# Kernel tuning notes

Hardware: AMD Instinct MI355X
Metric: run time of the kernel (lower is better)

The kernel has to match this reference:

```python
import jax, jax.numpy as jnp
import numpy as np

SEQ_LEN, BATCH, DIM = 4096, 16, 1024
MIN_SPAN = 8
MAX_SPAN = 200
LN_EPS = 1e-5

def _linear(x, w, b):
    return x @ w.T + b

def _layernorm(x, g, b):
    mu = jnp.mean(x, axis=-1, keepdims=True)
    var = jnp.var(x, axis=-1, keepdims=True)
    return (x - mu) * jax.lax.rsqrt(var + LN_EPS) * g + b

def _relevance_pool(hist, context, decay, w1, b1, w2, b2):
    # hist: [L,B,D], context: [B,D]; batched version of the per-sample torch loop
    L = hist.shape[0]
    ctx = jnp.broadcast_to(context[None], (L,) + context.shape)
    comb = jnp.concatenate([hist, ctx], axis=-1)                      # [L,B,2D]
    h = jax.nn.gelu(_linear(comb, w1, b1), approximate=False)
    scores = _linear(h, w2, b2)[..., 0]                               # [L,B]
    pos = jnp.arange(L, dtype=hist.dtype)
    dec = decay ** (L - 1 - pos)                                      # temporal decay, newest=1
    w = jax.nn.softmax(scores + jnp.log(dec + 1e-8)[:, None], axis=0) # softmax over time
    return jnp.einsum('lb,lbd->bd', w, hist)                          # [B,D]

def setup_inputs() -> dict:
    key = jax.random.key(0)
    ks = jax.random.split(key, 12)
    D, H = DIM, DIM // 2
    s = lambda k, shape, fan: jax.random.normal(k, shape, jnp.float32) * (1.0 / np.sqrt(fan))
    return {
        'features': jax.random.normal(ks[0], (SEQ_LEN, BATCH, D), jnp.float32),
        'w_sp1': s(ks[1], (H, D), D), 'b_sp1': jnp.zeros((H,), jnp.float32),
        'w_sp2': s(ks[2], (3, H), H), 'b_sp2': jnp.zeros((3,), jnp.float32),
        'w_rs1': s(ks[3], (H, 2 * D), 2 * D), 'b_rs1': jnp.zeros((H,), jnp.float32),
        'w_rs2': s(ks[4], (1, H), H), 'b_rs2': jnp.zeros((1,), jnp.float32),
        'decay_local': jnp.array(0.9, jnp.float32),
        'decay_global': jnp.array(0.8, jnp.float32),
        'w_ff': s(ks[5], (D, 2 * D), 2 * D), 'b_ff': jnp.zeros((D,), jnp.float32),
        'ln_ff_g': jnp.ones((D,), jnp.float32), 'ln_ff_b': jnp.zeros((D,), jnp.float32),
        'w_gate': s(ks[6], (D, D), D), 'b_gate': jnp.zeros((D,), jnp.float32),
        'ln_g': jnp.ones((D,), jnp.float32), 'ln_b': jnp.zeros((D,), jnp.float32),
    }

def reference(features, w_sp1, b_sp1, w_sp2, b_sp2, w_rs1, b_rs1, w_rs2, b_rs2,
              decay_local, decay_global, w_ff, b_ff, ln_ff_g, ln_ff_b,
              w_gate, b_gate, ln_g, ln_b):
    S, B, D = features.shape
    context = jnp.mean(features, axis=0)                              # [B,D]
    sp_h = jax.nn.gelu(_linear(context, w_sp1, b_sp1), approximate=False)
    span_weights = jax.nn.softmax(_linear(sp_h, w_sp2, b_sp2), axis=-1)  # [B,3]

    local_span = min(MIN_SPAN * 4, S)                                 # 32
    local_hist = features[-local_span:]                               # [32,B,D]
    local_feat = _relevance_pool(local_hist, context, decay_local,
                                 w_rs1, b_rs1, w_rs2, b_rs2)          # [B,D]

    step = max(1, S // 32) if S > 32 else 1
    global_hist = features[::step]                                    # [~32,B,D]
    global_feat = _relevance_pool(global_hist, context, decay_global,
                                  w_rs1, b_rs1, w_rs2, b_rs2)         # [B,D]

    combined = jnp.concatenate([local_feat * span_weights[:, 1:2],
                                global_feat * span_weights[:, 2:3]], axis=-1)  # [B,2D]
    fused = _layernorm(jax.nn.gelu(_linear(combined, w_ff, b_ff), approximate=False),
                       ln_ff_g, ln_ff_b)                              # [B,D]

    fused_expanded = jnp.broadcast_to(fused[None], (S, B, D))
    gate = jax.nn.sigmoid(_linear(fused_expanded, w_gate, b_gate))    # [S,B,D]
    output = _layernorm(fused_expanded * gate + features, ln_g, ln_b)

    attention_weights = jnp.full((S, B), 1.0 / S, dtype=features.dtype)
    return output, attention_weights
```

## Files before the change

kernel.cpp:

```cpp
#include <hip/hip_runtime.h>
#include <hip/hip_bf16.h>

#define S_LEN 4096
#define BATCH 16
#define DIM 1024
#define HDIM 512
#define LPOOL 32
#define NCOL (BATCH * DIM)
#define NCOL4 (NCOL / 4)
#define SCHUNK 64
#define ROWS_PER_CHUNK (S_LEN / SCHUNK)
#define LN_EPS 1e-5f

__device__ __forceinline__ float gelu_exact(float x) {
    return 0.5f * x * (1.0f + erff(x * 0.70710678118654752440f));
}

__device__ __forceinline__ float wave_reduce_sum(float v) {
    #pragma unroll
    for (int off = 32; off > 0; off >>= 1) v += __shfl_down(v, off);
    return v;
}

__global__ void __launch_bounds__(256) k_colsum(const float* __restrict__ f,
                                                float* __restrict__ part) {
    int cb = blockIdx.x;
    int sc = blockIdx.y;
    int t  = threadIdx.x;
    int c4 = cb * 256 + t;
    const float4* f4 = (const float4*)f;
    float4 acc = make_float4(0.f, 0.f, 0.f, 0.f);
    int base = sc * ROWS_PER_CHUNK;
    #pragma unroll 4
    for (int i = 0; i < ROWS_PER_CHUNK; ++i) {
        float4 v = f4[(size_t)(base + i) * NCOL4 + c4];
        acc.x += v.x; acc.y += v.y; acc.z += v.z; acc.w += v.w;
    }
    ((float4*)part)[(size_t)sc * NCOL4 + c4] = acc;
}

__global__ void __launch_bounds__(256) k_ctx_reduce(const float* __restrict__ part,
                                                    float* __restrict__ context) {
    int c = blockIdx.x * 256 + threadIdx.x;
    float s = 0.f;
    #pragma unroll 8
    for (int k = 0; k < SCHUNK; ++k) s += part[(size_t)k * NCOL + c];
    context[c] = s * (1.0f / (float)S_LEN);
}

__global__ void k_transpose(const float* __restrict__ w, float* __restrict__ wT) {
    __shared__ float tile[32][33];
    int jt = blockIdx.x * 32;
    int dt = blockIdx.y * 32;
    int tx = threadIdx.x & 31, ty = threadIdx.x >> 5;
    #pragma unroll
    for (int i = 0; i < 32; i += 8)
        tile[ty + i][tx] = w[(size_t)(jt + ty + i) * 2048 + dt + tx];
    __syncthreads();
    #pragma unroll
    for (int i = 0; i < 32; i += 8)
        wT[(size_t)(dt + ty + i) * 512 + jt + tx] = tile[tx][ty + i];
}

__global__ void k_sph(const float* __restrict__ ctx, const float* __restrict__ w1,
                      const float* __restrict__ b1, float* __restrict__ sph) {
    int wid = blockIdx.x * 4 + (threadIdx.x >> 6);
    int lane = threadIdx.x & 63;
    int b = wid >> 9;
    int j = wid & 511;
    const float4* x4 = (const float4*)(ctx + (size_t)b * DIM);
    const float4* w4 = (const float4*)(w1 + (size_t)j * DIM);
    float s = 0.f;
    #pragma unroll
    for (int i = 0; i < 4; ++i) {
        float4 a = x4[lane + i * 64], w = w4[lane + i * 64];
        s += a.x * w.x + a.y * w.y + a.z * w.z + a.w * w.w;
    }
    s = wave_reduce_sum(s);
    if (lane == 0) sph[b * HDIM + j] = gelu_exact(s + b1[j]);
}

__global__ void k_span(const float* __restrict__ sph, const float* __restrict__ w2,
                       const float* __restrict__ b2, float* __restrict__ spanw) {
    int b = blockIdx.x, lane = threadIdx.x;
    float vals[3];
    #pragma unroll
    for (int k = 0; k < 3; ++k) {
        const float4* x4 = (const float4*)(sph + (size_t)b * HDIM);
        const float4* w4 = (const float4*)(w2 + (size_t)k * HDIM);
        float s = 0.f;
        #pragma unroll
        for (int i = 0; i < 2; ++i) {
            float4 a = x4[lane + i * 64], w = w4[lane + i * 64];
            s += a.x * w.x + a.y * w.y + a.z * w.z + a.w * w.w;
        }
        s = wave_reduce_sum(s);
        vals[k] = s;
    }
    if (lane == 0) {
        float l0 = vals[0] + b2[0], l1 = vals[1] + b2[1], l2 = vals[2] + b2[2];
        float m = fmaxf(l0, fmaxf(l1, l2));
        float e0 = expf(l0 - m), e1 = expf(l1 - m), e2 = expf(l2 - m);
        float inv = 1.0f / (e0 + e1 + e2);
        spanw[b * 3 + 0] = e0 * inv;
        spanw[b * 3 + 1] = e1 * inv;
        spanw[b * 3 + 2] = e2 * inv;
    }
}

__global__ void k_ctxpart(const float* __restrict__ ctx, const float* __restrict__ wrs1,
                          const float* __restrict__ brs1, float* __restrict__ cpart) {
    int wid = blockIdx.x * 4 + (threadIdx.x >> 6);
    int lane = threadIdx.x & 63;
    int b = wid >> 9;
    int j = wid & 511;
    const float4* x4 = (const float4*)(ctx + (size_t)b * DIM);
    const float4* w4 = (const float4*)(wrs1 + (size_t)j * 2048 + 1024);
    float s = 0.f;
    #pragma unroll
    for (int i = 0; i < 4; ++i) {
        float4 a = x4[lane + i * 64], w = w4[lane + i * 64];
        s += a.x * w.x + a.y * w.y + a.z * w.z + a.w * w.w;
    }
    s = wave_reduce_sum(s);
    if (lane == 0) cpart[b * HDIM + j] = s + brs1[j];
}

__global__ void __launch_bounds__(256) k_poolh(const float* __restrict__ feat,
                                               const float* __restrict__ wT,
                                               const float* __restrict__ cpart,
                                               float* __restrict__ hws) {
    int pl = blockIdx.x;
    int p = pl >> 5, l = pl & 31;
    int jq = blockIdx.y;
    int s = (p == 0) ? (S_LEN - LPOOL + l) : (l * (S_LEN / 32));
    __shared__ float hist[BATCH * DIM];
    const float4* src4 = (const float4*)(feat + (size_t)s * NCOL);
    float4* h4 = (float4*)hist;
    #pragma unroll
    for (int i = 0; i < 16; ++i) h4[threadIdx.x + i * 256] = src4[threadIdx.x + i * 256];
    __syncthreads();
    int lane = threadIdx.x & 63;
    int b0 = (threadIdx.x >> 6) * 4;
    int j0 = jq * 128 + lane * 2;
    float acc[4][2];
    #pragma unroll
    for (int k = 0; k < 4; ++k) {
        acc[k][0] = cpart[(b0 + k) * HDIM + j0];
        acc[k][1] = cpart[(b0 + k) * HDIM + j0 + 1];
    }
    #pragma unroll 4
    for (int d = 0; d < DIM; ++d) {
        float2 w = *(const float2*)&wT[(size_t)d * HDIM + j0];
        #pragma unroll
        for (int k = 0; k < 4; ++k) {
            float h = hist[(b0 + k) * DIM + d];
            acc[k][0] += h * w.x;
            acc[k][1] += h * w.y;
        }
    }
    #pragma unroll
    for (int k = 0; k < 4; ++k) {
        int b = b0 + k;
        float2 o = make_float2(gelu_exact(acc[k][0]), gelu_exact(acc[k][1]));
        *(float2*)&hws[(((size_t)pl) * BATCH + b) * HDIM + j0] = o;
    }
}

__global__ void k_pool_finish(const float* __restrict__ feat, const float* __restrict__ hws,
                              const float* __restrict__ wrs2, const float* __restrict__ brs2,
                              const float* __restrict__ spanw, const float* __restrict__ dl,
                              const float* __restrict__ dg, float* __restrict__ combined) {
    int p = blockIdx.x >> 4, b = blockIdx.x & 15;
    int t = threadIdx.x, lane = t & 63, w = t >> 6;
    __shared__ float sc[LPOOL];
    __shared__ float wl[LPOOL];
    for (int li = w; li < LPOOL; li += 4) {
        const float4* h4 = (const float4*)(hws + (((size_t)(p * LPOOL + li)) * BATCH + b) * HDIM);
        const float4* w4 = (const float4*)wrs2;
        float s = 0.f;
        #pragma unroll
        for (int i = 0; i < 2; ++i) {
            float4 a = h4[lane + i * 64], ww = w4[lane + i * 64];
            s += a.x * ww.x + a.y * ww.y + a.z * ww.z + a.w * ww.w;
        }
        s = wave_reduce_sum(s);
        if (lane == 0) sc[li] = s + brs2[0];
    }
    __syncthreads();
    if (t == 0) {
        float decay = (p == 0) ? dl[0] : dg[0];
        float lg[LPOOL];
        float m = -1e30f;
        #pragma unroll
        for (int li = 0; li < LPOOL; ++li) {
            lg[li] = sc[li] + logf(powf(decay, (float)(LPOOL - 1 - li)) + 1e-8f);
            m = fmaxf(m, lg[li]);
        }
        float sum = 0.f;
        #pragma unroll
        for (int li = 0; li < LPOOL; ++li) { lg[li] = expf(lg[li] - m); sum += lg[li]; }
        float inv = 1.0f / sum;
        #pragma unroll
        for (int li = 0; li < LPOOL; ++li) wl[li] = lg[li] * inv;
    }
    __syncthreads();
    float sw = spanw[b * 3 + 1 + p];
    float4 acc = make_float4(0.f, 0.f, 0.f, 0.f);
    for (int li = 0; li < LPOOL; ++li) {
        int s_idx = (p == 0) ? (S_LEN - LPOOL + li) : (li * (S_LEN / 32));
        float4 v = ((const float4*)(feat + ((size_t)s_idx * BATCH + b) * DIM))[t];
        float wv = wl[li];
        acc.x += wv * v.x; acc.y += wv * v.y; acc.z += wv * v.z; acc.w += wv * v.w;
    }
    acc.x *= sw; acc.y *= sw; acc.z *= sw; acc.w *= sw;
    ((float4*)(combined + (size_t)b * 2048 + p * DIM))[t] = acc;
}

__global__ void k_ff(const float* __restrict__ comb, const float* __restrict__ wff,
                     const float* __restrict__ bff, float* __restrict__ ffout) {
    int wid = blockIdx.x * 4 + (threadIdx.x >> 6);
    int lane = threadIdx.x & 63;
    int b = wid >> 10, j = wid & 1023;
    const float4* x4 = (const float4*)(comb + (size_t)b * 2048);
    const float4* w4 = (const float4*)(wff + (size_t)j * 2048);
    float s = 0.f;
    #pragma unroll
    for (int i = 0; i < 8; ++i) {
        float4 a = x4[lane + i * 64], w = w4[lane + i * 64];
        s += a.x * w.x + a.y * w.y + a.z * w.z + a.w * w.w;
    }
    s = wave_reduce_sum(s);
    if (lane == 0) ffout[b * DIM + j] = gelu_exact(s + bff[j]);
}

__device__ __forceinline__ float2 block_sum2(float a, float bsum) {
    __shared__ float sa[4], sb[4];
    int lane = threadIdx.x & 63, w = threadIdx.x >> 6;
    #pragma unroll
    for (int off = 32; off > 0; off >>= 1) {
        a += __shfl_down(a, off);
        bsum += __shfl_down(bsum, off);
    }
    if (lane == 0) { sa[w] = a; sb[w] = bsum; }
    __syncthreads();
    float ta = sa[0] + sa[1] + sa[2] + sa[3];
    float tb = sb[0] + sb[1] + sb[2] + sb[3];
    return make_float2(ta, tb);
}

__global__ void k_ln_ff(const float* __restrict__ ffout, const float* __restrict__ g,
                        const float* __restrict__ bb, float* __restrict__ fused) {
    int b = blockIdx.x, t = threadIdx.x;
    float4 y = ((const float4*)(ffout + (size_t)b * DIM))[t];
    float s = y.x + y.y + y.z + y.w;
    float ss = y.x * y.x + y.y * y.y + y.z * y.z + y.w * y.w;
    float2 tot = block_sum2(s, ss);
    float mu = tot.x * (1.0f / DIM);
    float var = tot.y * (1.0f / DIM) - mu * mu;
    float rs = rsqrtf(var + LN_EPS);
    float4 g4 = ((const float4*)g)[t], b4 = ((const float4*)bb)[t];
    float4 o;
    o.x = (y.x - mu) * rs * g4.x + b4.x;
    o.y = (y.y - mu) * rs * g4.y + b4.y;
    o.z = (y.z - mu) * rs * g4.z + b4.z;
    o.w = (y.w - mu) * rs * g4.w + b4.w;
    ((float4*)(fused + (size_t)b * DIM))[t] = o;
}

__global__ void k_gate(const float* __restrict__ fused, const float* __restrict__ wg,
                       const float* __restrict__ bg, float* __restrict__ fg) {
    int wid = blockIdx.x * 4 + (threadIdx.x >> 6);
    int lane = threadIdx.x & 63;
    int b = wid >> 10, j = wid & 1023;
    const float4* x4 = (const float4*)(fused + (size_t)b * DIM);
    const float4* w4 = (const float4*)(wg + (size_t)j * DIM);
    float s = 0.f;
    #pragma unroll
    for (int i = 0; i < 4; ++i) {
        float4 a = x4[lane + i * 64], w = w4[lane + i * 64];
        s += a.x * w.x + a.y * w.y + a.z * w.z + a.w * w.w;
    }
    s = wave_reduce_sum(s);
    if (lane == 0) {
        float gv = 1.0f / (1.0f + expf(-(s + bg[j])));
        fg[b * DIM + j] = fused[b * DIM + j] * gv;
    }
}

__global__ void __launch_bounds__(256) k_final(const float* __restrict__ feat,
                                               const float* __restrict__ fg,
                                               const float* __restrict__ g,
                                               const float* __restrict__ bb,
                                               float* __restrict__ out,
                                               float* __restrict__ attn) {
    int r = blockIdx.x;
    int b = r & 15;
    int t = threadIdx.x;
    float4 x = ((const float4*)feat)[(size_t)r * 256 + t];
    float4 f4 = ((const float4*)(fg + (size_t)b * DIM))[t];
    float4 y;
    y.x = x.x + f4.x; y.y = x.y + f4.y; y.z = x.z + f4.z; y.w = x.w + f4.w;
    float s = y.x + y.y + y.z + y.w;
    float ss = y.x * y.x + y.y * y.y + y.z * y.z + y.w * y.w;
    float2 tot = block_sum2(s, ss);
    float mu = tot.x * (1.0f / DIM);
    float var = tot.y * (1.0f / DIM) - mu * mu;
    float rs = rsqrtf(var + LN_EPS);
    float4 g4 = ((const float4*)g)[t], bb4 = ((const float4*)bb)[t];
    float4 o;
    o.x = (y.x - mu) * rs * g4.x + bb4.x;
    o.y = (y.y - mu) * rs * g4.y + bb4.y;
    o.z = (y.z - mu) * rs * g4.z + bb4.z;
    o.w = (y.w - mu) * rs * g4.w + bb4.w;
    ((float4*)out)[(size_t)r * 256 + t] = o;
    if (t == 0) attn[r] = 1.0f / (float)S_LEN;
}

extern "C" void kernel_launch(void* const* d_in, const int* in_sizes, int n_in,
                              void* d_out, int out_size, void* d_ws, size_t ws_size,
                              hipStream_t stream) {
    const float* feat    = (const float*)d_in[0];
    const float* w_sp1   = (const float*)d_in[1];
    const float* b_sp1   = (const float*)d_in[2];
    const float* w_sp2   = (const float*)d_in[3];
    const float* b_sp2   = (const float*)d_in[4];
    const float* w_rs1   = (const float*)d_in[5];
    const float* b_rs1   = (const float*)d_in[6];
    const float* w_rs2   = (const float*)d_in[7];
    const float* b_rs2   = (const float*)d_in[8];
    const float* dl      = (const float*)d_in[9];
    const float* dg      = (const float*)d_in[10];
    const float* w_ff    = (const float*)d_in[11];
    const float* b_ff    = (const float*)d_in[12];
    const float* ln_ff_g = (const float*)d_in[13];
    const float* ln_ff_b = (const float*)d_in[14];
    const float* w_gate  = (const float*)d_in[15];
    const float* b_gate  = (const float*)d_in[16];
    const float* ln_g    = (const float*)d_in[17];
    const float* ln_b    = (const float*)d_in[18];

    float* out  = (float*)d_out;
    float* attn = out + (size_t)S_LEN * BATCH * DIM;

    float* ws = (float*)d_ws;
    float* part     = ws;
    float* wT       = ws;
    float* hws      = ws + 524288;
    float* context  = ws + 1048576;
    float* sph      = context + 16384;
    float* spanw    = sph + 8192;
    float* cpart    = spanw + 64;
    float* combined = cpart + 8192;
    float* ffout    = combined + 32768;
    float* fusedv   = ffout + 16384;
    float* fgv      = fusedv + 16384;

    k_colsum<<<dim3(16, 64), 256, 0, stream>>>(feat, part);
    k_ctx_reduce<<<64, 256, 0, stream>>>(part, context);
    k_transpose<<<dim3(16, 32), 256, 0, stream>>>(w_rs1, wT);
    k_sph<<<2048, 256, 0, stream>>>(context, w_sp1, b_sp1, sph);
    k_span<<<16, 64, 0, stream>>>(sph, w_sp2, b_sp2, spanw);
    k_ctxpart<<<2048, 256, 0, stream>>>(context, w_rs1, b_rs1, cpart);
    k_poolh<<<dim3(64, 4), 256, 0, stream>>>(feat, wT, cpart, hws);
    k_pool_finish<<<32, 256, 0, stream>>>(feat, hws, w_rs2, b_rs2, spanw, dl, dg, combined);
    k_ff<<<4096, 256, 0, stream>>>(combined, w_ff, b_ff, ffout);
    k_ln_ff<<<16, 256, 0, stream>>>(ffout, ln_ff_g, ln_ff_b, fusedv);
    k_gate<<<4096, 256, 0, stream>>>(fusedv, w_gate, b_gate, fgv);
    k_final<<<65536, 256, 0, stream>>>(feat, fgv, ln_g, ln_b, out, attn);
}
```

Measured before the change: 679.9 us.

## Batch GEMV kernels over all rows, merge small kernels, wave-per-row layernorm

The matrix-vector kernels (sph, ctx part, ff, gate) now give each wave one output column across all 16 batch rows, so each weight row is loaded once and reused 16 times instead of being re-read per batch. The context reduce and transpose are merged into one launch, and the sph and ctx part kernels into another. Both layernorm kernels switch from block-wide reductions with shared memory and a barrier to one wave per row using xor shuffles. The pool-h kernel uses 512 threads with fewer batch rows each, and the workspace layout is changed so the transposed weights no longer alias the partial sums. Holding 16 accumulators per thread raises register pressure.

```diff
diff --git a/kernel.cpp b/kernel.cpp
--- a/kernel.cpp
+++ b/kernel.cpp
@@ -16,9 +16,19 @@
     return 0.5f * x * (1.0f + erff(x * 0.70710678118654752440f));
 }
 
+__device__ __forceinline__ float dot4(float4 a, float4 b) {
+    return a.x * b.x + a.y * b.y + a.z * b.z + a.w * b.w;
+}
+
 __device__ __forceinline__ float wave_reduce_sum(float v) {
     #pragma unroll
     for (int off = 32; off > 0; off >>= 1) v += __shfl_down(v, off);
+    return v;
+}
+
+__device__ __forceinline__ float wave_allreduce_sum(float v) {
+    #pragma unroll
+    for (int off = 32; off > 0; off >>= 1) v += __shfl_xor(v, off);
     return v;
 }
 
@@ -39,45 +49,72 @@
     ((float4*)part)[(size_t)sc * NCOL4 + c4] = acc;
 }
 
-__global__ void __launch_bounds__(256) k_ctx_reduce(const float* __restrict__ part,
-                                                    float* __restrict__ context) {
-    int c = blockIdx.x * 256 + threadIdx.x;
-    float s = 0.f;
-    #pragma unroll 8
-    for (int k = 0; k < SCHUNK; ++k) s += part[(size_t)k * NCOL + c];
-    context[c] = s * (1.0f / (float)S_LEN);
-}
-
-__global__ void k_transpose(const float* __restrict__ w, float* __restrict__ wT) {
-    __shared__ float tile[32][33];
-    int jt = blockIdx.x * 32;
-    int dt = blockIdx.y * 32;
-    int tx = threadIdx.x & 31, ty = threadIdx.x >> 5;
-    #pragma unroll
-    for (int i = 0; i < 32; i += 8)
-        tile[ty + i][tx] = w[(size_t)(jt + ty + i) * 2048 + dt + tx];
-    __syncthreads();
-    #pragma unroll
-    for (int i = 0; i < 32; i += 8)
-        wT[(size_t)(dt + ty + i) * 512 + jt + tx] = tile[tx][ty + i];
-}
-
-__global__ void k_sph(const float* __restrict__ ctx, const float* __restrict__ w1,
-                      const float* __restrict__ b1, float* __restrict__ sph) {
+__global__ void __launch_bounds__(256) k_prep(const float* __restrict__ part,
+                                              float* __restrict__ context,
+                                              const float* __restrict__ w,
+                                              float* __restrict__ wT) {
+    if (blockIdx.x < 64) {
+        int c = blockIdx.x * 256 + threadIdx.x;
+        float s = 0.f;
+        #pragma unroll 8
+        for (int k = 0; k < SCHUNK; ++k) s += part[(size_t)k * NCOL + c];
+        context[c] = s * (1.0f / (float)S_LEN);
+    } else {
+        __shared__ float tile[32][33];
+        int t = blockIdx.x - 64;
+        int jt = (t & 15) * 32;
+        int dt = (t >> 4) * 32;
+        int tx = threadIdx.x & 31, ty = threadIdx.x >> 5;
+        #pragma unroll
+        for (int i = 0; i < 32; i += 8)
+            tile[ty + i][tx] = w[(size_t)(jt + ty + i) * 2048 + dt + tx];
+        __syncthreads();
+        #pragma unroll
+        for (int i = 0; i < 32; i += 8)
+            wT[(size_t)(dt + ty + i) * 512 + jt + tx] = tile[tx][ty + i];
+    }
+}
+
+__global__ void __launch_bounds__(256) k_sph_cpart(const float* __restrict__ ctx,
+                                                   const float* __restrict__ w_sp1,
+                                                   const float* __restrict__ b_sp1,
+                                                   const float* __restrict__ w_rs1,
+                                                   const float* __restrict__ b_rs1,
+                                                   float* __restrict__ sph,
+                                                   float* __restrict__ cpart) {
     int wid = blockIdx.x * 4 + (threadIdx.x >> 6);
     int lane = threadIdx.x & 63;
-    int b = wid >> 9;
-    int j = wid & 511;
-    const float4* x4 = (const float4*)(ctx + (size_t)b * DIM);
-    const float4* w4 = (const float4*)(w1 + (size_t)j * DIM);
-    float s = 0.f;
-    #pragma unroll
-    for (int i = 0; i < 4; ++i) {
-        float4 a = x4[lane + i * 64], w = w4[lane + i * 64];
-        s += a.x * w.x + a.y * w.y + a.z * w.z + a.w * w.w;
-    }
-    s = wave_reduce_sum(s);
-    if (lane == 0) sph[b * HDIM + j] = gelu_exact(s + b1[j]);
+    bool is_sph = (wid < 512);
+    int j = is_sph ? wid : (wid - 512);
+    const float4* w4 = is_sph ? (const float4*)(w_sp1 + (size_t)j * DIM)
+                              : (const float4*)(w_rs1 + (size_t)j * 2048 + 1024);
+    float acc[BATCH];
+    #pragma unroll
+    for (int b = 0; b < BATCH; ++b) acc[b] = 0.f;
+    #pragma unroll
+    for (int i = 0; i < 4; ++i) {
+        float4 w = w4[lane + i * 64];
+        #pragma unroll
+        for (int b = 0; b < BATCH; ++b) {
+            float4 x = ((const float4*)(ctx + (size_t)b * DIM))[lane + i * 64];
+            acc[b] += dot4(w, x);
+        }
+    }
+    #pragma unroll
+    for (int b = 0; b < BATCH; ++b) acc[b] = wave_reduce_sum(acc[b]);
+    if (lane == 0) {
+        if (is_sph) {
+            float bias = b_sp1[j];
+            #pragma unroll
+            for (int b = 0; b < BATCH; ++b)
+                sph[b * HDIM + j] = gelu_exact(acc[b] + bias);
+        } else {
+            float bias = b_rs1[j];
+            #pragma unroll
+            for (int b = 0; b < BATCH; ++b)
+                cpart[b * HDIM + j] = acc[b] + bias;
+        }
+    }
 }
 
 __global__ void k_span(const float* __restrict__ sph, const float* __restrict__ w2,
@@ -92,7 +129,7 @@
         #pragma unroll
         for (int i = 0; i < 2; ++i) {
             float4 a = x4[lane + i * 64], w = w4[lane + i * 64];
-            s += a.x * w.x + a.y * w.y + a.z * w.z + a.w * w.w;
+            s += dot4(a, w);
         }
         s = wave_reduce_sum(s);
         vals[k] = s;
@@ -108,25 +145,7 @@
     }
 }
 
-__global__ void k_ctxpart(const float* __restrict__ ctx, const float* __restrict__ wrs1,
-                          const float* __restrict__ brs1, float* __restrict__ cpart) {
-    int wid = blockIdx.x * 4 + (threadIdx.x >> 6);
-    int lane = threadIdx.x & 63;
-    int b = wid >> 9;
-    int j = wid & 511;
-    const float4* x4 = (const float4*)(ctx + (size_t)b * DIM);
-    const float4* w4 = (const float4*)(wrs1 + (size_t)j * 2048 + 1024);
-    float s = 0.f;
-    #pragma unroll
-    for (int i = 0; i < 4; ++i) {
-        float4 a = x4[lane + i * 64], w = w4[lane + i * 64];
-        s += a.x * w.x + a.y * w.y + a.z * w.z + a.w * w.w;
-    }
-    s = wave_reduce_sum(s);
-    if (lane == 0) cpart[b * HDIM + j] = s + brs1[j];
-}
-
-__global__ void __launch_bounds__(256) k_poolh(const float* __restrict__ feat,
+__global__ void __launch_bounds__(512) k_poolh(const float* __restrict__ feat,
                                                const float* __restrict__ wT,
                                                const float* __restrict__ cpart,
                                                float* __restrict__ hws) {
@@ -138,14 +157,14 @@
     const float4* src4 = (const float4*)(feat + (size_t)s * NCOL);
     float4* h4 = (float4*)hist;
     #pragma unroll
-    for (int i = 0; i < 16; ++i) h4[threadIdx.x + i * 256] = src4[threadIdx.x + i * 256];
+    for (int i = 0; i < 8; ++i) h4[threadIdx.x + i * 512] = src4[threadIdx.x + i * 512];
     __syncthreads();
     int lane = threadIdx.x & 63;
-    int b0 = (threadIdx.x >> 6) * 4;
+    int b0 = (threadIdx.x >> 6) * 2;
     int j0 = jq * 128 + lane * 2;
-    float acc[4][2];
-    #pragma unroll
-    for (int k = 0; k < 4; ++k) {
+    float acc[2][2];
+    #pragma unroll
+    for (int k = 0; k < 2; ++k) {
         acc[k][0] = cpart[(b0 + k) * HDIM + j0];
         acc[k][1] = cpart[(b0 + k) * HDIM + j0 + 1];
     }
@@ -153,14 +172,14 @@
     for (int d = 0; d < DIM; ++d) {
         float2 w = *(const float2*)&wT[(size_t)d * HDIM + j0];
         #pragma unroll
-        for (int k = 0; k < 4; ++k) {
+        for (int k = 0; k < 2; ++k) {
             float h = hist[(b0 + k) * DIM + d];
             acc[k][0] += h * w.x;
             acc[k][1] += h * w.y;
         }
     }
     #pragma unroll
-    for (int k = 0; k < 4; ++k) {
+    for (int k = 0; k < 2; ++k) {
         int b = b0 + k;
         float2 o = make_float2(gelu_exact(acc[k][0]), gelu_exact(acc[k][1]));
         *(float2*)&hws[(((size_t)pl) * BATCH + b) * HDIM + j0] = o;
@@ -182,7 +201,7 @@
         #pragma unroll
         for (int i = 0; i < 2; ++i) {
             float4 a = h4[lane + i * 64], ww = w4[lane + i * 64];
-            s += a.x * ww.x + a.y * ww.y + a.z * ww.z + a.w * ww.w;
+            s += dot4(a, ww);
         }
         s = wave_reduce_sum(s);
         if (lane == 0) sc[li] = s + brs2[0];
@@ -217,74 +236,98 @@
     ((float4*)(combined + (size_t)b * 2048 + p * DIM))[t] = acc;
 }
 
-__global__ void k_ff(const float* __restrict__ comb, const float* __restrict__ wff,
-                     const float* __restrict__ bff, float* __restrict__ ffout) {
-    int wid = blockIdx.x * 4 + (threadIdx.x >> 6);
-    int lane = threadIdx.x & 63;
-    int b = wid >> 10, j = wid & 1023;
-    const float4* x4 = (const float4*)(comb + (size_t)b * 2048);
+__global__ void __launch_bounds__(256) k_ff(const float* __restrict__ comb,
+                                            const float* __restrict__ wff,
+                                            const float* __restrict__ bff,
+                                            float* __restrict__ ffout) {
+    int j = blockIdx.x * 4 + (threadIdx.x >> 6);
+    int lane = threadIdx.x & 63;
     const float4* w4 = (const float4*)(wff + (size_t)j * 2048);
-    float s = 0.f;
+    float acc[BATCH];
+    #pragma unroll
+    for (int b = 0; b < BATCH; ++b) acc[b] = 0.f;
     #pragma unroll
     for (int i = 0; i < 8; ++i) {
-        float4 a = x4[lane + i * 64], w = w4[lane + i * 64];
-        s += a.x * w.x + a.y * w.y + a.z * w.z + a.w * w.w;
-    }
-    s = wave_reduce_sum(s);
-    if (lane == 0) ffout[b * DIM + j] = gelu_exact(s + bff[j]);
-}
-
-__device__ __forceinline__ float2 block_sum2(float a, float bsum) {
-    __shared__ float sa[4], sb[4];
-    int lane = threadIdx.x & 63, w = threadIdx.x >> 6;
-    #pragma unroll
-    for (int off = 32; off > 0; off >>= 1) {
-        a += __shfl_down(a, off);
-        bsum += __shfl_down(bsum, off);
-    }
-    if (lane == 0) { sa[w] = a; sb[w] = bsum; }
-    __syncthreads();
-    float ta = sa[0] + sa[1] + sa[2] + sa[3];
-    float tb = sb[0] + sb[1] + sb[2] + sb[3];
-    return make_float2(ta, tb);
-}
-
-__global__ void k_ln_ff(const float* __restrict__ ffout, const float* __restrict__ g,
-                        const float* __restrict__ bb, float* __restrict__ fused) {
-    int b = blockIdx.x, t = threadIdx.x;
-    float4 y = ((const float4*)(ffout + (size_t)b * DIM))[t];
-    float s = y.x + y.y + y.z + y.w;
-    float ss = y.x * y.x + y.y * y.y + y.z * y.z + y.w * y.w;
-    float2 tot = block_sum2(s, ss);
-    float mu = tot.x * (1.0f / DIM);
-    float var = tot.y * (1.0f / DIM) - mu * mu;
+        float4 w = w4[lane + i * 64];
+        #pragma unroll
+        for (int b = 0; b < BATCH; ++b) {
+            float4 x = ((const float4*)(comb + (size_t)b * 2048))[lane + i * 64];
+            acc[b] += dot4(w, x);
+        }
+    }
+    #pragma unroll
+    for (int b = 0; b < BATCH; ++b) acc[b] = wave_reduce_sum(acc[b]);
+    if (lane == 0) {
+        float bias = bff[j];
+        #pragma unroll
+        for (int b = 0; b < BATCH; ++b)
+            ffout[b * DIM + j] = gelu_exact(acc[b] + bias);
+    }
+}
+
+__global__ void __launch_bounds__(256) k_ln_ff(const float* __restrict__ ffout,
+                                               const float* __restrict__ g,
+                                               const float* __restrict__ bb,
+                                               float* __restrict__ fused) {
+    int b = blockIdx.x * 4 + (threadIdx.x >> 6);
+    int lane = threadIdx.x & 63;
+    const float4* row = (const float4*)ffout + (size_t)b * 256;
+    float4 y[4];
+    float s = 0.f, ss = 0.f;
+    #pragma unroll
+    for (int i = 0; i < 4; ++i) {
+        float4 v = row[lane + i * 64];
+        y[i] = v;
+        s += v.x + v.y + v.z + v.w;
+        ss += v.x * v.x + v.y * v.y + v.z * v.z + v.w * v.w;
+    }
+    s = wave_allreduce_sum(s);
+    ss = wave_allreduce_sum(ss);
+    float mu = s * (1.0f / DIM);
+    float var = ss * (1.0f / DIM) - mu * mu;
     float rs = rsqrtf(var + LN_EPS);
-    float4 g4 = ((const float4*)g)[t], b4 = ((const float4*)bb)[t];
-    float4 o;
-    o.x = (y.x - mu) * rs * g4.x + b4.x;
-    o.y = (y.y - mu) * rs * g4.y + b4.y;
-    o.z = (y.z - mu) * rs * g4.z + b4.z;
-    o.w = (y.w - mu) * rs * g4.w + b4.w;
-    ((float4*)(fused + (size_t)b * DIM))[t] = o;
-}
-
-__global__ void k_gate(const float* __restrict__ fused, const float* __restrict__ wg,
-                       const float* __restrict__ bg, float* __restrict__ fg) {
-    int wid = blockIdx.x * 4 + (threadIdx.x >> 6);
-    int lane = threadIdx.x & 63;
-    int b = wid >> 10, j = wid & 1023;
-    const float4* x4 = (const float4*)(fused + (size_t)b * DIM);
+    float4* orow = (float4*)fused + (size_t)b * 256;
+    #pragma unroll
+    for (int i = 0; i < 4; ++i) {
+        float4 g4 = ((const float4*)g)[lane + i * 64];
+        float4 b4 = ((const float4*)bb)[lane + i * 64];
+        float4 o;
+        o.x = (y[i].x - mu) * rs * g4.x + b4.x;
+        o.y = (y[i].y - mu) * rs * g4.y + b4.y;
+        o.z = (y[i].z - mu) * rs * g4.z + b4.z;
+        o.w = (y[i].w - mu) * rs * g4.w + b4.w;
+        orow[lane + i * 64] = o;
+    }
+}
+
+__global__ void __launch_bounds__(256) k_gate(const float* __restrict__ fused,
+                                              const float* __restrict__ wg,
+                                              const float* __restrict__ bg,
+                                              float* __restrict__ fg) {
+    int j = blockIdx.x * 4 + (threadIdx.x >> 6);
+    int lane = threadIdx.x & 63;
     const float4* w4 = (const float4*)(wg + (size_t)j * DIM);
-    float s = 0.f;
-    #pragma unroll
-    for (int i = 0; i < 4; ++i) {
-        float4 a = x4[lane + i * 64], w = w4[lane + i * 64];
-        s += a.x * w.x + a.y * w.y + a.z * w.z + a.w * w.w;
-    }
-    s = wave_reduce_sum(s);
+    float acc[BATCH];
+    #pragma unroll
+    for (int b = 0; b < BATCH; ++b) acc[b] = 0.f;
+    #pragma unroll
+    for (int i = 0; i < 4; ++i) {
+        float4 w = w4[lane + i * 64];
+        #pragma unroll
+        for (int b = 0; b < BATCH; ++b) {
+            float4 x = ((const float4*)(fused + (size_t)b * DIM))[lane + i * 64];
+            acc[b] += dot4(w, x);
+        }
+    }
+    #pragma unroll
+    for (int b = 0; b < BATCH; ++b) acc[b] = wave_reduce_sum(acc[b]);
     if (lane == 0) {
-        float gv = 1.0f / (1.0f + expf(-(s + bg[j])));
-        fg[b * DIM + j] = fused[b * DIM + j] * gv;
+        float bias = bg[j];
+        #pragma unroll
+        for (int b = 0; b < BATCH; ++b) {
+            float gv = 1.0f / (1.0f + expf(-(acc[b] + bias)));
+            fg[b * DIM + j] = fused[b * DIM + j] * gv;
+        }
     }
 }
 
@@ -294,27 +337,41 @@
                                                const float* __restrict__ bb,
                                                float* __restrict__ out,
                                                float* __restrict__ attn) {
-    int r = blockIdx.x;
+    int r = blockIdx.x * 4 + (threadIdx.x >> 6);
+    int lane = threadIdx.x & 63;
     int b = r & 15;
-    int t = threadIdx.x;
-    float4 x = ((const float4*)feat)[(size_t)r * 256 + t];
-    float4 f4 = ((const float4*)(fg + (size_t)b * DIM))[t];
-    float4 y;
-    y.x = x.x + f4.x; y.y = x.y + f4.y; y.z = x.z + f4.z; y.w = x.w + f4.w;
-    float s = y.x + y.y + y.z + y.w;
-    float ss = y.x * y.x + y.y * y.y + y.z * y.z + y.w * y.w;
-    float2 tot = block_sum2(s, ss);
-    float mu = tot.x * (1.0f / DIM);
-    float var = tot.y * (1.0f / DIM) - mu * mu;
+    const float4* xrow = (const float4*)feat + (size_t)r * 256;
+    const float4* frow = (const float4*)fg + (size_t)b * 256;
+    float4 y[4];
+    float s = 0.f, ss = 0.f;
+    #pragma unroll
+    for (int i = 0; i < 4; ++i) {
+        float4 x = xrow[lane + i * 64];
+        float4 f = frow[lane + i * 64];
+        float4 v;
+        v.x = x.x + f.x; v.y = x.y + f.y; v.z = x.z + f.z; v.w = x.w + f.w;
+        y[i] = v;
+        s += v.x + v.y + v.z + v.w;
+        ss += v.x * v.x + v.y * v.y + v.z * v.z + v.w * v.w;
+    }
+    s = wave_allreduce_sum(s);
+    ss = wave_allreduce_sum(ss);
+    float mu = s * (1.0f / DIM);
+    float var = ss * (1.0f / DIM) - mu * mu;
     float rs = rsqrtf(var + LN_EPS);
-    float4 g4 = ((const float4*)g)[t], bb4 = ((const float4*)bb)[t];
-    float4 o;
-    o.x = (y.x - mu) * rs * g4.x + bb4.x;
-    o.y = (y.y - mu) * rs * g4.y + bb4.y;
-    o.z = (y.z - mu) * rs * g4.z + bb4.z;
-    o.w = (y.w - mu) * rs * g4.w + bb4.w;
-    ((float4*)out)[(size_t)r * 256 + t] = o;
-    if (t == 0) attn[r] = 1.0f / (float)S_LEN;
+    float4* orow = (float4*)out + (size_t)r * 256;
+    #pragma unroll
+    for (int i = 0; i < 4; ++i) {
+        float4 g4 = ((const float4*)g)[lane + i * 64];
+        float4 b4 = ((const float4*)bb)[lane + i * 64];
+        float4 o;
+        o.x = (y[i].x - mu) * rs * g4.x + b4.x;
+        o.y = (y[i].y - mu) * rs * g4.y + b4.y;
+        o.z = (y[i].z - mu) * rs * g4.z + b4.z;
+        o.w = (y[i].w - mu) * rs * g4.w + b4.w;
+        orow[lane + i * 64] = o;
+    }
+    if (lane == 0) attn[r] = 1.0f / (float)S_LEN;
 }
 
 extern "C" void kernel_launch(void* const* d_in, const int* in_sizes, int n_in,
@@ -345,9 +402,9 @@
 
     float* ws = (float*)d_ws;
     float* part     = ws;
-    float* wT       = ws;
-    float* hws      = ws + 524288;
-    float* context  = ws + 1048576;
+    float* wT       = ws + 1048576;
+    float* hws      = wT + 524288;
+    float* context  = hws + 524288;
     float* sph      = context + 16384;
     float* spanw    = sph + 8192;
     float* cpart    = spanw + 64;
@@ -357,15 +414,13 @@
     float* fgv      = fusedv + 16384;
 
     k_colsum<<<dim3(16, 64), 256, 0, stream>>>(feat, part);
-    k_ctx_reduce<<<64, 256, 0, stream>>>(part, context);
-    k_transpose<<<dim3(16, 32), 256, 0, stream>>>(w_rs1, wT);
-    k_sph<<<2048, 256, 0, stream>>>(context, w_sp1, b_sp1, sph);
+    k_prep<<<576, 256, 0, stream>>>(part, context, w_rs1, wT);
+    k_sph_cpart<<<256, 256, 0, stream>>>(context, w_sp1, b_sp1, w_rs1, b_rs1, sph, cpart);
     k_span<<<16, 64, 0, stream>>>(sph, w_sp2, b_sp2, spanw);
-    k_ctxpart<<<2048, 256, 0, stream>>>(context, w_rs1, b_rs1, cpart);
-    k_poolh<<<dim3(64, 4), 256, 0, stream>>>(feat, wT, cpart, hws);
+    k_poolh<<<dim3(64, 4), 512, 0, stream>>>(feat, wT, cpart, hws);
     k_pool_finish<<<32, 256, 0, stream>>>(feat, hws, w_rs2, b_rs2, spanw, dl, dg, combined);
-    k_ff<<<4096, 256, 0, stream>>>(combined, w_ff, b_ff, ffout);
-    k_ln_ff<<<16, 256, 0, stream>>>(ffout, ln_ff_g, ln_ff_b, fusedv);
-    k_gate<<<4096, 256, 0, stream>>>(fusedv, w_gate, b_gate, fgv);
-    k_final<<<65536, 256, 0, stream>>>(feat, fgv, ln_g, ln_b, out, attn);
-}
+    k_ff<<<256, 256, 0, stream>>>(combined, w_ff, b_ff, ffout);
+    k_ln_ff<<<4, 256, 0, stream>>>(ffout, ln_ff_g, ln_ff_b, fusedv);
+    k_gate<<<256, 256, 0, stream>>>(fusedv, w_gate, b_gate, fgv);
+    k_final<<<16384, 256, 0, stream>>>(feat, fgv, ln_g, ln_b, out, attn);
+}
```

Result: slower. 723.0 us (+6.3%).
